# Kernel tuning notes

Measured on AMD Instinct MI355X. Metric: run time of the kernel, lower is better.

Reference implementation:

```python
import jax, jax.numpy as jnp
import numpy as np
from math import pi as PI

N_NODES = 50000
N_EDGES = 1000000
HIDDEN = 128
N_GAUSS = 50
N_FILT = 128
N_COLORS = 4
CUTOFF = 10.0
LOG2 = float(np.log(2.0))


def setup_inputs() -> dict:
    key = jax.random.key(0)
    ks = jax.random.split(key, 16)
    glorot = jax.nn.initializers.glorot_uniform()
    inp = {
        "x": jax.random.normal(ks[0], (N_NODES, HIDDEN), jnp.float32),
        "edge_index": jax.random.randint(ks[1], (2, N_EDGES), 0, N_NODES),
        "edge_weight": jax.random.uniform(ks[2], (N_EDGES,), jnp.float32) * CUTOFF,
        "edge_attr": jax.random.normal(ks[3], (N_EDGES, N_GAUSS), jnp.float32),
        "colors": jax.random.randint(ks[4], (N_EDGES,), 0, N_COLORS),
        # ColoredMLP params, stacked over colors
        "mlp1_w": glorot(ks[5], (N_COLORS, N_FILT, N_GAUSS), jnp.float32),
        "mlp1_b": jnp.zeros((N_COLORS, N_FILT), jnp.float32),
        "mlp2_w": glorot(ks[6], (N_COLORS, N_FILT, N_FILT), jnp.float32),
        "mlp2_b": jnp.zeros((N_COLORS, N_FILT), jnp.float32),
        # CFConv linears
        "lin1_w": glorot(ks[7], (N_FILT, HIDDEN), jnp.float32),
        "lin2_w": glorot(ks[8], (HIDDEN, N_FILT), jnp.float32),
        "lin2_b": jnp.zeros((HIDDEN,), jnp.float32),
        # final Linear
        "lin_w": glorot(ks[9], (HIDDEN, HIDDEN), jnp.float32),
        "lin_b": jnp.zeros((HIDDEN,), jnp.float32),
    }
    return inp


def shifted_softplus(v):
    return jax.nn.softplus(v) - LOG2


def colored_mlp(edge_attr, colors, mlp1_w, mlp1_b, mlp2_w, mlp2_b):
    # per-color small MLP; loop over the small fixed color set, select by mask
    out = jnp.zeros((edge_attr.shape[0], N_FILT), edge_attr.dtype)
    for c in range(N_COLORS):
        h = shifted_softplus(edge_attr @ mlp1_w[c].T + mlp1_b[c])
        h = h @ mlp2_w[c].T + mlp2_b[c]
        out = jnp.where((colors == c)[:, None], h, out)
    return out


def reference(x, edge_index, edge_weight, edge_attr, colors,
              mlp1_w, mlp1_b, mlp2_w, mlp2_b,
              lin1_w, lin2_w, lin2_b, lin_w, lin_b):
    # cosine cutoff
    C = 0.5 * (jnp.cos(edge_weight * PI / CUTOFF) + 1.0)  # [E]
    W = colored_mlp(edge_attr, colors, mlp1_w, mlp1_b, mlp2_w, mlp2_b) * C[:, None]  # [E,F]
    h = x @ lin1_w.T  # [N,F]
    src, dst = edge_index[0], edge_index[1]
    msg = h[src] * W  # gather + modulate, [E,F]
    agg = jax.ops.segment_sum(msg, dst, num_segments=N_NODES)  # scatter-add, [N,F]
    out = agg @ lin2_w.T + lin2_b  # [N,H]
    out = shifted_softplus(out)
    out = out @ lin_w.T + lin_b
    return out
```

## Files before the change

### kernel.cpp

```cpp
#include <hip/hip_runtime.h>
#include <math.h>

#define N_NODES_ 50000
#define N_EDGES_ 1000000
#define HID 128
#define NG 50
#define NF 128
#define NCOL 4
#define CSEG 258048
#define NKEY (NCOL * N_NODES_)
#define CHUNK 625
#define NCHUNK_PER_C 80
#define NCHUNK (NCOL * NCHUNK_PER_C)

typedef short s16x8 __attribute__((ext_vector_type(8)));
typedef float f32x4 __attribute__((ext_vector_type(4)));

__device__ __forceinline__ float sspf(float v) {
    float r = __logf(1.f + __expf(v)) - 0.69314718055994531f;
    return (v > 15.f) ? (v - 0.69314718055994531f) : r;
}

__device__ __forceinline__ unsigned int f2b(float f) {
    unsigned int u = __float_as_uint(f);
    return (u + 0x7fffu + ((u >> 16) & 1u)) >> 16;
}

template <int CTRL>
__device__ __forceinline__ float dpp_shl_f(float v) {
    return __int_as_float(__builtin_amdgcn_update_dpp(
        0, __float_as_int(v), CTRL, 0xF, 0xF, false));
}

__global__ __launch_bounds__(256) void hist_kernel(const int* __restrict__ colors,
                                                   const int* __restrict__ edge_index,
                                                   int* __restrict__ hist) {
    int e = blockIdx.x * 256 + threadIdx.x;
    if (e < N_EDGES_) {
        int key = colors[e] * N_NODES_ + edge_index[N_EDGES_ + e];
        atomicAdd(&hist[key], 1);
    }
}

__global__ __launch_bounds__(256) void scan1_kernel(int* __restrict__ hist,
                                                    int* __restrict__ csum) {
    __shared__ int s[CHUNK];
    int b = blockIdx.x;
    int c = b / NCHUNK_PER_C, ch = b % NCHUNK_PER_C;
    int gofs = c * N_NODES_ + ch * CHUNK;
    for (int i = threadIdx.x; i < CHUNK; i += 256) s[i] = hist[gofs + i];
    __syncthreads();
    if (threadIdx.x == 0) {
        int run = 0;
        for (int i = 0; i < CHUNK; ++i) { int t = s[i]; s[i] = run; run += t; }
        csum[b] = run;
    }
    __syncthreads();
    for (int i = threadIdx.x; i < CHUNK; i += 256) hist[gofs + i] = s[i];
}

__global__ __launch_bounds__(64) void scan2_kernel(const int* __restrict__ csum,
                                                   int* __restrict__ cbase,
                                                   int* __restrict__ g_cnt) {
    int c = threadIdx.x;
    if (c < NCOL) {
        int run = 0;
        for (int j = 0; j < NCHUNK_PER_C; ++j) {
            cbase[c * NCHUNK_PER_C + j] = run;
            run += csum[c * NCHUNK_PER_C + j];
        }
        g_cnt[c] = run;
    }
}

__global__ __launch_bounds__(256) void scan3_kernel(int* __restrict__ hist,
                                                    const int* __restrict__ cbase) {
    int b = blockIdx.x;
    int c = b / NCHUNK_PER_C, ch = b % NCHUNK_PER_C;
    int gofs = c * N_NODES_ + ch * CHUNK;
    int add = cbase[b];
    for (int i = threadIdx.x; i < CHUNK; i += 256) hist[gofs + i] += add;
}

__global__ __launch_bounds__(256) void fill_kernel(int* __restrict__ erec) {
    int i = blockIdx.x * 256 + threadIdx.x;
    if (i < NCOL * CSEG) {
        erec[3 * i + 0] = -1;
        erec[3 * i + 1] = (int)0xFFFF0000u;
        erec[3 * i + 2] = 0;
    }
}

__global__ __launch_bounds__(256) void scatter_kernel(const int* __restrict__ colors,
                                                      const int* __restrict__ edge_index,
                                                      const float* __restrict__ edge_weight,
                                                      int* __restrict__ base,
                                                      int* __restrict__ erec) {
    int e = blockIdx.x * 256 + threadIdx.x;
    if (e < N_EDGES_) {
        int c = colors[e];
        int d = edge_index[N_EDGES_ + e];
        int s = edge_index[e];
        int key = c * N_NODES_ + d;
        int r = atomicAdd(&base[key], 1);
        float cwv = 0.5f * (__cosf(edge_weight[e] * 0.31415926535897932f) + 1.f);
        size_t slot = (size_t)(c * CSEG + r) * 3;
        erec[slot + 0] = e;
        erec[slot + 1] = (int)(((unsigned)d << 16) | (unsigned)s);
        erec[slot + 2] = (int)__float_as_uint(cwv);
    }
}

__global__ __launch_bounds__(256) void wconv_kernel(const float* __restrict__ m1w,
                                                    const float* __restrict__ m2w,
                                                    unsigned short* __restrict__ m1b16,
                                                    unsigned short* __restrict__ m2b16) {
    int idx = blockIdx.x * 256 + threadIdx.x;
    if (idx < NCOL * NF * 64) {
        int c = idx / (NF * 64);
        int rem = idx % (NF * 64);
        int n = rem / 64, k = rem % 64;
        float v = (k < NG) ? m1w[(c * NF + n) * NG + k] : 0.f;
        m1b16[idx] = (unsigned short)f2b(v);
    } else if (idx < NCOL * NF * 64 + NCOL * NF * NF) {
        int j = idx - NCOL * NF * 64;
        int cn = j / NF;
        int k = j % NF;
        int ks = k >> 5, qk = (k >> 3) & 3, jj = k & 7;
        int tau = ((2 * ks + (jj >> 2)) << 4) | (qk << 2) | (jj & 3);
        m2b16[j] = (unsigned short)f2b(m2w[cn * NF + tau]);
    }
}

__global__ __launch_bounds__(256, 4) void passA_kernel(
    const float* __restrict__ edge_attr,
    const unsigned short* __restrict__ m1b16, const unsigned short* __restrict__ m2b16,
    const float* __restrict__ m1bias, const float* __restrict__ m2bias,
    const float* __restrict__ h, const int* __restrict__ erec,
    const int* __restrict__ g_cnt, float* __restrict__ agg) {

    __shared__ __align__(16) char sm2[32768];

    int c = blockIdx.x >> 12;
    int tile = blockIdx.x & 4095;
    int cnt = g_cnt[c];
    if (tile * 64 >= cnt) return;
    int pos0 = c * CSEG + tile * 64;

    int tid = threadIdx.x;
    int wv = tid >> 6;
    int l15 = tid & 15;
    int q = (tid >> 4) & 3;
    int e = (wv << 4) | l15;

    {
        const uint4* g4 = (const uint4*)(m2b16 + (size_t)c * NF * NF);
#pragma unroll
        for (int i = 0; i < 8; ++i) {
            int c0 = tid + 256 * i;
            int row = c0 >> 4;
            int k0 = c0 & 15;
            int dstb = row * 256 + ((k0 * 16) ^ ((row & 7) << 4));
            *(uint4*)(sm2 + dstb) = g4[c0];
        }
    }

    size_t ri = (size_t)(pos0 + e) * 3;
    int eid = erec[ri + 0];
    unsigned w1 = (unsigned)erec[ri + 1];
    float cw = __int_as_float(erec[ri + 2]);
    int d = (int)(w1 >> 16);
    int sidx = (int)(w1 & 0xFFFFu);

    union { s16x8 v; unsigned int u[4]; } bf0, bf1;
    {
        const float* ear = edge_attr + (size_t)((eid >= 0) ? eid : 0) * NG;
        float2 a0 = *(const float2*)(ear + q * 8 + 0);
        float2 a1 = *(const float2*)(ear + q * 8 + 2);
        float2 a2v = *(const float2*)(ear + q * 8 + 4);
        float2 a3 = *(const float2*)(ear + q * 8 + 6);
        bf0.u[0] = f2b(a0.x) | (f2b(a0.y) << 16);
        bf0.u[1] = f2b(a1.x) | (f2b(a1.y) << 16);
        bf0.u[2] = f2b(a2v.x) | (f2b(a2v.y) << 16);
        bf0.u[3] = f2b(a3.x) | (f2b(a3.y) << 16);
        float2 c0 = make_float2(0.f, 0.f), c1 = c0, c2 = c0, c3 = c0;
        int k1 = 32 + q * 8;
        if (q < 2) {
            c0 = *(const float2*)(ear + k1 + 0);
            c1 = *(const float2*)(ear + k1 + 2);
            c2 = *(const float2*)(ear + k1 + 4);
            c3 = *(const float2*)(ear + k1 + 6);
        } else if (q == 2) {
            c0 = *(const float2*)(ear + 48);
        }
        bf1.u[0] = f2b(c0.x) | (f2b(c0.y) << 16);
        bf1.u[1] = f2b(c1.x) | (f2b(c1.y) << 16);
        bf1.u[2] = f2b(c2.x) | (f2b(c2.y) << 16);
        bf1.u[3] = f2b(c3.x) | (f2b(c3.y) << 16);
    }

    f32x4 acc1[8];
    {
        const unsigned short* m1p = m1b16 + (size_t)c * NF * 64;
#pragma unroll
        for (int m = 0; m < 8; ++m) {
            f32x4 z = (f32x4)(0.f);
            s16x8 af0 = *(const s16x8*)(m1p + (m * 16 + l15) * 64 + q * 8);
            acc1[m] = __builtin_amdgcn_mfma_f32_16x16x32_bf16(af0, bf0.v, z, 0, 0, 0);
        }
#pragma unroll
        for (int m = 0; m < 8; ++m) {
            s16x8 af1 = *(const s16x8*)(m1p + (m * 16 + l15) * 64 + q * 8 + 32);
            acc1[m] = __builtin_amdgcn_mfma_f32_16x16x32_bf16(af1, bf1.v, acc1[m], 0, 0, 0);
        }
    }

    uint2 p[8];
    {
        const float* b1p = m1bias + c * NF;
#pragma unroll
        for (int m = 0; m < 8; ++m) {
            int n0 = m * 16 + q * 4;
            f32x4 bv = *(const f32x4*)(b1p + n0);
            float t0 = sspf(acc1[m][0] + bv[0]);
            float t1 = sspf(acc1[m][1] + bv[1]);
            float t2 = sspf(acc1[m][2] + bv[2]);
            float t3 = sspf(acc1[m][3] + bv[3]);
            p[m].x = f2b(t0) | (f2b(t1) << 16);
            p[m].y = f2b(t2) | (f2b(t3) << 16);
        }
    }

    int dprev = __shfl_up(d, 1, 16);
    int dn1 = __shfl_down(d, 1, 16);
    int dn2 = __shfl_down(d, 2, 16);
    int dn4 = __shfl_down(d, 4, 16);
    int dn8 = __shfl_down(d, 8, 16);
    float f1 = ((dn1 == d) && (l15 + 1 < 16)) ? 1.f : 0.f;
    float f2 = ((dn2 == d) && (l15 + 2 < 16)) ? 1.f : 0.f;
    float f4 = ((dn4 == d) && (l15 + 4 < 16)) ? 1.f : 0.f;
    float f8 = ((dn8 == d) && (l15 + 8 < 16)) ? 1.f : 0.f;
    bool head = (eid >= 0) && (l15 == 0 || d != dprev);

    __syncthreads();

    const float* hrow = h + (size_t)sidx * HID;
    f32x4 hv[8];
#pragma unroll
    for (int m = 0; m < 8; ++m) hv[m] = *(const f32x4*)(hrow + m * 16 + q * 4);

    f32x4 a2[8];
#pragma unroll
    for (int m = 0; m < 8; ++m) a2[m] = (f32x4)(0.f);
    {
        int rowb0 = l15 * 256;
        int sw = (l15 & 7) << 4;
#pragma unroll
        for (int ks = 0; ks < 4; ++ks) {
            union { s16x8 v; unsigned int u[4]; } bfr;
            bfr.u[0] = p[2 * ks].x;
            bfr.u[1] = p[2 * ks].y;
            bfr.u[2] = p[2 * ks + 1].x;
            bfr.u[3] = p[2 * ks + 1].y;
            int off = (q * 16 + ks * 64) ^ sw;
#pragma unroll
            for (int m = 0; m < 8; ++m) {
                s16x8 af = *(const s16x8*)(sm2 + rowb0 + m * 4096 + off);
                a2[m] = __builtin_amdgcn_mfma_f32_16x16x32_bf16(af, bfr.v, a2[m], 0, 0, 0);
            }
        }
    }

    {
        const float* b2p = m2bias + c * NF;
#pragma unroll
        for (int m = 0; m < 8; ++m) {
            int n0 = m * 16 + q * 4;
            f32x4 bv = *(const f32x4*)(b2p + n0);
            a2[m][0] = (a2[m][0] + bv[0]) * cw * hv[m][0];
            a2[m][1] = (a2[m][1] + bv[1]) * cw * hv[m][1];
            a2[m][2] = (a2[m][2] + bv[2]) * cw * hv[m][2];
            a2[m][3] = (a2[m][3] + bv[3]) * cw * hv[m][3];
        }
    }

#pragma unroll
    for (int m = 0; m < 8; ++m) {
#pragma unroll
        for (int j = 0; j < 4; ++j) {
            float x = a2[m][j];
            x = fmaf(f1, dpp_shl_f<0x101>(x), x);
            x = fmaf(f2, dpp_shl_f<0x102>(x), x);
            x = fmaf(f4, dpp_shl_f<0x104>(x), x);
            x = fmaf(f8, dpp_shl_f<0x108>(x), x);
            a2[m][j] = x;
        }
    }

    if (head) {
        float* ap = agg + (size_t)d * HID + (q << 2);
#pragma unroll
        for (int m = 0; m < 8; ++m) {
            atomicAdd(ap + m * 16 + 0, a2[m][0]);
            atomicAdd(ap + m * 16 + 1, a2[m][1]);
            atomicAdd(ap + m * 16 + 2, a2[m][2]);
            atomicAdd(ap + m * 16 + 3, a2[m][3]);
        }
    }
}

__device__ __forceinline__ void fma_2x8(float (&acc)[2][8], float2 a, float4 b0, float4 b1) {
    acc[0][0] += a.x * b0.x; acc[0][1] += a.x * b0.y;
    acc[0][2] += a.x * b0.z; acc[0][3] += a.x * b0.w;
    acc[0][4] += a.x * b1.x; acc[0][5] += a.x * b1.y;
    acc[0][6] += a.x * b1.z; acc[0][7] += a.x * b1.w;
    acc[1][0] += a.y * b0.x; acc[1][1] += a.y * b0.y;
    acc[1][2] += a.y * b0.z; acc[1][3] += a.y * b0.w;
    acc[1][4] += a.y * b1.x; acc[1][5] += a.y * b1.y;
    acc[1][6] += a.y * b1.z; acc[1][7] += a.y * b1.w;
}

__device__ __forceinline__ void load_wT32(const float4* __restrict__ w4, int kc,
                                          float (*wT)[132], int tid) {
#pragma unroll
    for (int i = 0; i < 4; ++i) {
        int lin = tid + 256 * i;
        int col = lin >> 3;
        int m = lin & 7;
        float4 v = w4[col * 32 + (kc >> 2) + m];
        wT[4 * m + 0][col] = v.x;
        wT[4 * m + 1][col] = v.y;
        wT[4 * m + 2][col] = v.z;
        wT[4 * m + 3][col] = v.w;
    }
}

__global__ __launch_bounds__(256) void lin1_kernel(const float* __restrict__ x,
                                                   const float* __restrict__ w,
                                                   float* __restrict__ h) {
    __shared__ float xT[HID][36];
    __shared__ float wT[32][132];
    int tid = threadIdx.x;
    int tx = tid & 15, ty = tid >> 4;
    int r0 = blockIdx.x * 32;
    const float4* x4 = (const float4*)x;
#pragma unroll
    for (int i = 0; i < 4; ++i) {
        int lin = tid + 256 * i;
        int r = lin >> 5, m = lin & 31;
        int rr = r0 + r; if (rr > N_NODES_ - 1) rr = N_NODES_ - 1;
        float4 v = x4[rr * 32 + m];
        xT[4 * m + 0][r] = v.x; xT[4 * m + 1][r] = v.y;
        xT[4 * m + 2][r] = v.z; xT[4 * m + 3][r] = v.w;
    }
    float acc[2][8] = {};
    for (int kc = 0; kc < HID; kc += 32) {
        __syncthreads();
        load_wT32((const float4*)w, kc, wT, tid);
        __syncthreads();
#pragma unroll 8
        for (int k2 = 0; k2 < 32; ++k2) {
            float2 a = *(const float2*)&xT[kc + k2][2 * ty];
            float4 b0 = *(const float4*)&wT[k2][8 * tx];
            float4 b1 = *(const float4*)&wT[k2][8 * tx + 4];
            fma_2x8(acc, a, b0, b1);
        }
    }
    float4* h4 = (float4*)h;
#pragma unroll
    for (int i = 0; i < 2; ++i) {
        int row = r0 + 2 * ty + i;
        if (row < N_NODES_) {
            h4[row * 32 + 2 * tx]     = make_float4(acc[i][0], acc[i][1], acc[i][2], acc[i][3]);
            h4[row * 32 + 2 * tx + 1] = make_float4(acc[i][4], acc[i][5], acc[i][6], acc[i][7]);
        }
    }
}

__global__ __launch_bounds__(256) void out_kernel(
    const float* __restrict__ agg,
    const float* __restrict__ w2, const float* __restrict__ b2,
    const float* __restrict__ w3, const float* __restrict__ b3,
    float* __restrict__ out) {
    __shared__ float sT[HID][36];
    __shared__ float wT[32][132];
    int tid = threadIdx.x;
    int tx = tid & 15, ty = tid >> 4;
    int r0 = blockIdx.x * 32;
    const float4* a4 = (const float4*)agg;
#pragma unroll
    for (int i = 0; i < 4; ++i) {
        int lin = tid + 256 * i;
        int r = lin >> 5, m = lin & 31;
        int rr = r0 + r; if (rr > N_NODES_ - 1) rr = N_NODES_ - 1;
        float4 v = a4[rr * 32 + m];
        sT[4 * m + 0][r] = v.x; sT[4 * m + 1][r] = v.y;
        sT[4 * m + 2][r] = v.z; sT[4 * m + 3][r] = v.w;
    }
    float acc[2][8] = {};
    for (int kc = 0; kc < HID; kc += 32) {
        __syncthreads();
        load_wT32((const float4*)w2, kc, wT, tid);
        __syncthreads();
#pragma unroll 8
        for (int k2 = 0; k2 < 32; ++k2) {
            float2 a = *(const float2*)&sT[kc + k2][2 * ty];
            float4 c0 = *(const float4*)&wT[k2][8 * tx];
            float4 c1 = *(const float4*)&wT[k2][8 * tx + 4];
            fma_2x8(acc, a, c0, c1);
        }
    }
    __syncthreads();
#pragma unroll
    for (int j = 0; j < 8; ++j) {
        int col = 8 * tx + j;
        float bbv = b2[col];
        sT[col][2 * ty]     = sspf(acc[0][j] + bbv);
        sT[col][2 * ty + 1] = sspf(acc[1][j] + bbv);
    }
    float acc2[2][8] = {};
    for (int kc = 0; kc < HID; kc += 32) {
        __syncthreads();
        load_wT32((const float4*)w3, kc, wT, tid);
        __syncthreads();
#pragma unroll 8
        for (int k2 = 0; k2 < 32; ++k2) {
            float2 a = *(const float2*)&sT[kc + k2][2 * ty];
            float4 c0 = *(const float4*)&wT[k2][8 * tx];
            float4 c1 = *(const float4*)&wT[k2][8 * tx + 4];
            fma_2x8(acc2, a, c0, c1);
        }
    }
    float4* out4 = (float4*)out;
#pragma unroll
    for (int i = 0; i < 2; ++i) {
        int row = r0 + 2 * ty + i;
        if (row < N_NODES_) {
            out4[row * 32 + 2 * tx] = make_float4(
                acc2[i][0] + b3[8 * tx + 0], acc2[i][1] + b3[8 * tx + 1],
                acc2[i][2] + b3[8 * tx + 2], acc2[i][3] + b3[8 * tx + 3]);
            out4[row * 32 + 2 * tx + 1] = make_float4(
                acc2[i][4] + b3[8 * tx + 4], acc2[i][5] + b3[8 * tx + 5],
                acc2[i][6] + b3[8 * tx + 6], acc2[i][7] + b3[8 * tx + 7]);
        }
    }
}

extern "C" void kernel_launch(void* const* d_in, const int* in_sizes, int n_in,
                              void* d_out, int out_size, void* d_ws, size_t ws_size,
                              hipStream_t stream) {
    const float* x           = (const float*)d_in[0];
    const int*   edge_index  = (const int*)d_in[1];
    const float* edge_weight = (const float*)d_in[2];
    const float* edge_attr   = (const float*)d_in[3];
    const int*   colors      = (const int*)d_in[4];
    const float* m1w         = (const float*)d_in[5];
    const float* m1b         = (const float*)d_in[6];
    const float* m2w         = (const float*)d_in[7];
    const float* m2b         = (const float*)d_in[8];
    const float* lin1w       = (const float*)d_in[9];
    const float* lin2w       = (const float*)d_in[10];
    const float* lin2b       = (const float*)d_in[11];
    const float* linw        = (const float*)d_in[12];
    const float* linb        = (const float*)d_in[13];
    float* out = (float*)d_out;

    char* ws = (char*)d_ws;
    float* h      = (float*)(ws);
    float* agg    = (float*)(ws + 25600000);
    int*   erec   = (int*)(ws + 51200000);
    int*   base   = (int*)(ws + 63586304);
    int*   csum   = (int*)(ws + 64386304);
    int*   cbase  = (int*)(ws + 64387584);
    int*   g_cnt  = (int*)(ws + 64388864);
    unsigned short* m1b16 = (unsigned short*)(ws + 64388928);
    unsigned short* m2b16 = (unsigned short*)(ws + 64454464);

    hipMemsetAsync(agg, 0, (size_t)N_NODES_ * HID * sizeof(float), stream);
    hipMemsetAsync(base, 0, NKEY * sizeof(int), stream);

    fill_kernel<<<(NCOL * CSEG + 255) / 256, 256, 0, stream>>>(erec);
    hist_kernel<<<(N_EDGES_ + 255) / 256, 256, 0, stream>>>(colors, edge_index, base);
    scan1_kernel<<<NCHUNK, 256, 0, stream>>>(base, csum);
    scan2_kernel<<<1, 64, 0, stream>>>(csum, cbase, g_cnt);
    scan3_kernel<<<NCHUNK, 256, 0, stream>>>(base, cbase);
    scatter_kernel<<<(N_EDGES_ + 255) / 256, 256, 0, stream>>>(colors, edge_index, edge_weight,
                                                               base, erec);
    wconv_kernel<<<(NCOL * NF * 64 + NCOL * NF * NF + 255) / 256, 256, 0, stream>>>(m1w, m2w, m1b16, m2b16);
    lin1_kernel<<<(N_NODES_ + 31) / 32, 256, 0, stream>>>(x, lin1w, h);
    passA_kernel<<<NCOL * 4096, 256, 0, stream>>>(edge_attr, m1b16, m2b16, m1b, m2b,
                                                  h, erec, g_cnt, agg);
    out_kernel<<<(N_NODES_ + 31) / 32, 256, 0, stream>>>(agg, lin2w, lin2b, linw, linb, out);
}
```

Baseline: 958.8 us.

## Make passA persistent per color and fold memsets into fill kernel

passA now launches a fixed 512 blocks per color, and each block loops over 64-edge tiles with a grid stride. The per-color layer-2 weights are staged into shared memory once per block instead of once per tile, and empty blocks are no longer launched. The two hipMemsetAsync calls for agg and base are folded into fill_kernel to drop separate launches, and the passA occupancy hint rises from 4 to 5 blocks per SIMD/CU. The risks are register pressure under the tighter launch bound and load imbalance across colors.

```diff
diff --git a/kernel.cpp b/kernel.cpp
--- a/kernel.cpp
+++ b/kernel.cpp
@@ -12,6 +12,7 @@
 #define CHUNK 625
 #define NCHUNK_PER_C 80
 #define NCHUNK (NCOL * NCHUNK_PER_C)
+#define BLKS_PER_C 512
 
 typedef short s16x8 __attribute__((ext_vector_type(8)));
 typedef float f32x4 __attribute__((ext_vector_type(4)));
@@ -82,13 +83,19 @@
     for (int i = threadIdx.x; i < CHUNK; i += 256) hist[gofs + i] += add;
 }
 
-__global__ __launch_bounds__(256) void fill_kernel(int* __restrict__ erec) {
+__global__ __launch_bounds__(256) void fill_kernel(int* __restrict__ erec,
+                                                   int* __restrict__ base,
+                                                   float4* __restrict__ agg4) {
     int i = blockIdx.x * 256 + threadIdx.x;
+    int nthr = gridDim.x * 256;
     if (i < NCOL * CSEG) {
         erec[3 * i + 0] = -1;
         erec[3 * i + 1] = (int)0xFFFF0000u;
         erec[3 * i + 2] = 0;
     }
+    if (i < NKEY) base[i] = 0;
+    for (int j = i; j < N_NODES_ * HID / 4; j += nthr)
+        agg4[j] = make_float4(0.f, 0.f, 0.f, 0.f);
 }
 
 __global__ __launch_bounds__(256) void scatter_kernel(const int* __restrict__ colors,
@@ -132,7 +139,7 @@
     }
 }
 
-__global__ __launch_bounds__(256, 4) void passA_kernel(
+__global__ __launch_bounds__(256, 5) void passA_kernel(
     const float* __restrict__ edge_attr,
     const unsigned short* __restrict__ m1b16, const unsigned short* __restrict__ m2b16,
     const float* __restrict__ m1bias, const float* __restrict__ m2bias,
@@ -141,11 +148,10 @@
 
     __shared__ __align__(16) char sm2[32768];
 
-    int c = blockIdx.x >> 12;
-    int tile = blockIdx.x & 4095;
+    int c = blockIdx.x >> 9;
+    int bslot = blockIdx.x & (BLKS_PER_C - 1);
     int cnt = g_cnt[c];
-    if (tile * 64 >= cnt) return;
-    int pos0 = c * CSEG + tile * 64;
+    int ntiles = (cnt + 63) >> 6;
 
     int tid = threadIdx.x;
     int wv = tid >> 6;
@@ -164,44 +170,52 @@
             *(uint4*)(sm2 + dstb) = g4[c0];
         }
     }
-
-    size_t ri = (size_t)(pos0 + e) * 3;
-    int eid = erec[ri + 0];
-    unsigned w1 = (unsigned)erec[ri + 1];
-    float cw = __int_as_float(erec[ri + 2]);
-    int d = (int)(w1 >> 16);
-    int sidx = (int)(w1 & 0xFFFFu);
-
-    union { s16x8 v; unsigned int u[4]; } bf0, bf1;
-    {
-        const float* ear = edge_attr + (size_t)((eid >= 0) ? eid : 0) * NG;
-        float2 a0 = *(const float2*)(ear + q * 8 + 0);
-        float2 a1 = *(const float2*)(ear + q * 8 + 2);
-        float2 a2v = *(const float2*)(ear + q * 8 + 4);
-        float2 a3 = *(const float2*)(ear + q * 8 + 6);
-        bf0.u[0] = f2b(a0.x) | (f2b(a0.y) << 16);
-        bf0.u[1] = f2b(a1.x) | (f2b(a1.y) << 16);
-        bf0.u[2] = f2b(a2v.x) | (f2b(a2v.y) << 16);
-        bf0.u[3] = f2b(a3.x) | (f2b(a3.y) << 16);
-        float2 c0 = make_float2(0.f, 0.f), c1 = c0, c2 = c0, c3 = c0;
-        int k1 = 32 + q * 8;
-        if (q < 2) {
-            c0 = *(const float2*)(ear + k1 + 0);
-            c1 = *(const float2*)(ear + k1 + 2);
-            c2 = *(const float2*)(ear + k1 + 4);
-            c3 = *(const float2*)(ear + k1 + 6);
-        } else if (q == 2) {
-            c0 = *(const float2*)(ear + 48);
-        }
-        bf1.u[0] = f2b(c0.x) | (f2b(c0.y) << 16);
-        bf1.u[1] = f2b(c1.x) | (f2b(c1.y) << 16);
-        bf1.u[2] = f2b(c2.x) | (f2b(c2.y) << 16);
-        bf1.u[3] = f2b(c3.x) | (f2b(c3.y) << 16);
-    }
-
-    f32x4 acc1[8];
-    {
-        const unsigned short* m1p = m1b16 + (size_t)c * NF * 64;
+    __syncthreads();
+
+    const unsigned short* m1p = m1b16 + (size_t)c * NF * 64;
+    const float* b1p = m1bias + c * NF;
+    const float* b2p = m2bias + c * NF;
+    int rowb0 = l15 * 256;
+    int sw = (l15 & 7) << 4;
+
+    for (int tile = bslot; tile < ntiles; tile += BLKS_PER_C) {
+        int pos0 = c * CSEG + tile * 64;
+
+        size_t ri = (size_t)(pos0 + e) * 3;
+        int eid = erec[ri + 0];
+        unsigned w1 = (unsigned)erec[ri + 1];
+        float cw = __int_as_float(erec[ri + 2]);
+        int d = (int)(w1 >> 16);
+        int sidx = (int)(w1 & 0xFFFFu);
+
+        union { s16x8 v; unsigned int u[4]; } bf0, bf1;
+        {
+            const float* ear = edge_attr + (size_t)((eid >= 0) ? eid : 0) * NG;
+            float2 a0 = *(const float2*)(ear + q * 8 + 0);
+            float2 a1 = *(const float2*)(ear + q * 8 + 2);
+            float2 a2v = *(const float2*)(ear + q * 8 + 4);
+            float2 a3 = *(const float2*)(ear + q * 8 + 6);
+            bf0.u[0] = f2b(a0.x) | (f2b(a0.y) << 16);
+            bf0.u[1] = f2b(a1.x) | (f2b(a1.y) << 16);
+            bf0.u[2] = f2b(a2v.x) | (f2b(a2v.y) << 16);
+            bf0.u[3] = f2b(a3.x) | (f2b(a3.y) << 16);
+            float2 c0 = make_float2(0.f, 0.f), c1 = c0, c2 = c0, c3 = c0;
+            int k1 = 32 + q * 8;
+            if (q < 2) {
+                c0 = *(const float2*)(ear + k1 + 0);
+                c1 = *(const float2*)(ear + k1 + 2);
+                c2 = *(const float2*)(ear + k1 + 4);
+                c3 = *(const float2*)(ear + k1 + 6);
+            } else if (q == 2) {
+                c0 = *(const float2*)(ear + 48);
+            }
+            bf1.u[0] = f2b(c0.x) | (f2b(c0.y) << 16);
+            bf1.u[1] = f2b(c1.x) | (f2b(c1.y) << 16);
+            bf1.u[2] = f2b(c2.x) | (f2b(c2.y) << 16);
+            bf1.u[3] = f2b(c3.x) | (f2b(c3.y) << 16);
+        }
+
+        f32x4 acc1[8];
 #pragma unroll
         for (int m = 0; m < 8; ++m) {
             f32x4 z = (f32x4)(0.f);
@@ -213,11 +227,8 @@
             s16x8 af1 = *(const s16x8*)(m1p + (m * 16 + l15) * 64 + q * 8 + 32);
             acc1[m] = __builtin_amdgcn_mfma_f32_16x16x32_bf16(af1, bf1.v, acc1[m], 0, 0, 0);
         }
-    }
-
-    uint2 p[8];
-    {
-        const float* b1p = m1bias + c * NF;
+
+        uint2 p[8];
 #pragma unroll
         for (int m = 0; m < 8; ++m) {
             int n0 = m * 16 + q * 4;
@@ -229,32 +240,26 @@
             p[m].x = f2b(t0) | (f2b(t1) << 16);
             p[m].y = f2b(t2) | (f2b(t3) << 16);
         }
-    }
-
-    int dprev = __shfl_up(d, 1, 16);
-    int dn1 = __shfl_down(d, 1, 16);
-    int dn2 = __shfl_down(d, 2, 16);
-    int dn4 = __shfl_down(d, 4, 16);
-    int dn8 = __shfl_down(d, 8, 16);
-    float f1 = ((dn1 == d) && (l15 + 1 < 16)) ? 1.f : 0.f;
-    float f2 = ((dn2 == d) && (l15 + 2 < 16)) ? 1.f : 0.f;
-    float f4 = ((dn4 == d) && (l15 + 4 < 16)) ? 1.f : 0.f;
-    float f8 = ((dn8 == d) && (l15 + 8 < 16)) ? 1.f : 0.f;
-    bool head = (eid >= 0) && (l15 == 0 || d != dprev);
-
-    __syncthreads();
-
-    const float* hrow = h + (size_t)sidx * HID;
-    f32x4 hv[8];
-#pragma unroll
-    for (int m = 0; m < 8; ++m) hv[m] = *(const f32x4*)(hrow + m * 16 + q * 4);
-
-    f32x4 a2[8];
-#pragma unroll
-    for (int m = 0; m < 8; ++m) a2[m] = (f32x4)(0.f);
-    {
-        int rowb0 = l15 * 256;
-        int sw = (l15 & 7) << 4;
+
+        int dprev = __shfl_up(d, 1, 16);
+        int dn1 = __shfl_down(d, 1, 16);
+        int dn2 = __shfl_down(d, 2, 16);
+        int dn4 = __shfl_down(d, 4, 16);
+        int dn8 = __shfl_down(d, 8, 16);
+        float f1 = ((dn1 == d) && (l15 + 1 < 16)) ? 1.f : 0.f;
+        float f2v = ((dn2 == d) && (l15 + 2 < 16)) ? 1.f : 0.f;
+        float f4 = ((dn4 == d) && (l15 + 4 < 16)) ? 1.f : 0.f;
+        float f8 = ((dn8 == d) && (l15 + 8 < 16)) ? 1.f : 0.f;
+        bool head = (eid >= 0) && (l15 == 0 || d != dprev);
+
+        const float* hrow = h + (size_t)sidx * HID;
+        f32x4 hv[8];
+#pragma unroll
+        for (int m = 0; m < 8; ++m) hv[m] = *(const f32x4*)(hrow + m * 16 + q * 4);
+
+        f32x4 a2[8];
+#pragma unroll
+        for (int m = 0; m < 8; ++m) a2[m] = (f32x4)(0.f);
 #pragma unroll
         for (int ks = 0; ks < 4; ++ks) {
             union { s16x8 v; unsigned int u[4]; } bfr;
@@ -269,10 +274,7 @@
                 a2[m] = __builtin_amdgcn_mfma_f32_16x16x32_bf16(af, bfr.v, a2[m], 0, 0, 0);
             }
         }
-    }
-
-    {
-        const float* b2p = m2bias + c * NF;
+
 #pragma unroll
         for (int m = 0; m < 8; ++m) {
             int n0 = m * 16 + q * 4;
@@ -282,29 +284,29 @@
             a2[m][2] = (a2[m][2] + bv[2]) * cw * hv[m][2];
             a2[m][3] = (a2[m][3] + bv[3]) * cw * hv[m][3];
         }
-    }
-
-#pragma unroll
-    for (int m = 0; m < 8; ++m) {
-#pragma unroll
-        for (int j = 0; j < 4; ++j) {
-            float x = a2[m][j];
-            x = fmaf(f1, dpp_shl_f<0x101>(x), x);
-            x = fmaf(f2, dpp_shl_f<0x102>(x), x);
-            x = fmaf(f4, dpp_shl_f<0x104>(x), x);
-            x = fmaf(f8, dpp_shl_f<0x108>(x), x);
-            a2[m][j] = x;
-        }
-    }
-
-    if (head) {
-        float* ap = agg + (size_t)d * HID + (q << 2);
+
 #pragma unroll
         for (int m = 0; m < 8; ++m) {
-            atomicAdd(ap + m * 16 + 0, a2[m][0]);
-            atomicAdd(ap + m * 16 + 1, a2[m][1]);
-            atomicAdd(ap + m * 16 + 2, a2[m][2]);
-            atomicAdd(ap + m * 16 + 3, a2[m][3]);
+#pragma unroll
+            for (int j = 0; j < 4; ++j) {
+                float x = a2[m][j];
+                x = fmaf(f1, dpp_shl_f<0x101>(x), x);
+                x = fmaf(f2v, dpp_shl_f<0x102>(x), x);
+                x = fmaf(f4, dpp_shl_f<0x104>(x), x);
+                x = fmaf(f8, dpp_shl_f<0x108>(x), x);
+                a2[m][j] = x;
+            }
+        }
+
+        if (head) {
+            float* ap = agg + (size_t)d * HID + (q << 2);
+#pragma unroll
+            for (int m = 0; m < 8; ++m) {
+                atomicAdd(ap + m * 16 + 0, a2[m][0]);
+                atomicAdd(ap + m * 16 + 1, a2[m][1]);
+                atomicAdd(ap + m * 16 + 2, a2[m][2]);
+                atomicAdd(ap + m * 16 + 3, a2[m][3]);
+            }
         }
     }
 }
@@ -476,10 +478,7 @@
     unsigned short* m1b16 = (unsigned short*)(ws + 64388928);
     unsigned short* m2b16 = (unsigned short*)(ws + 64454464);
 
-    hipMemsetAsync(agg, 0, (size_t)N_NODES_ * HID * sizeof(float), stream);
-    hipMemsetAsync(base, 0, NKEY * sizeof(int), stream);
-
-    fill_kernel<<<(NCOL * CSEG + 255) / 256, 256, 0, stream>>>(erec);
+    fill_kernel<<<(NCOL * CSEG + 255) / 256, 256, 0, stream>>>(erec, base, (float4*)agg);
     hist_kernel<<<(N_EDGES_ + 255) / 256, 256, 0, stream>>>(colors, edge_index, base);
     scan1_kernel<<<NCHUNK, 256, 0, stream>>>(base, csum);
     scan2_kernel<<<1, 64, 0, stream>>>(csum, cbase, g_cnt);
@@ -488,7 +487,7 @@
                                                                base, erec);
     wconv_kernel<<<(NCOL * NF * 64 + NCOL * NF * NF + 255) / 256, 256, 0, stream>>>(m1w, m2w, m1b16, m2b16);
     lin1_kernel<<<(N_NODES_ + 31) / 32, 256, 0, stream>>>(x, lin1w, h);
-    passA_kernel<<<NCOL * 4096, 256, 0, stream>>>(edge_attr, m1b16, m2b16, m1b, m2b,
-                                                  h, erec, g_cnt, agg);
+    passA_kernel<<<NCOL * BLKS_PER_C, 256, 0, stream>>>(edge_attr, m1b16, m2b16, m1b, m2b,
+                                                        h, erec, g_cnt, agg);
     out_kernel<<<(N_NODES_ + 31) / 32, 256, 0, stream>>>(agg, lin2w, lin2b, linw, linb, out);
 }
```

Result: slower. 1.513 ms (+57.8%).
